# Kernel tuning notes

Measured on AMD Instinct MI355X. Metric: run time of the kernel, lower is better.

Reference implementation:

```python
import jax, jax.numpy as jnp
import numpy as np

BN_EPS = 1e-5
C = 128  # channels (hardcoded by feed_forward convs)


def _bn(v, gamma, beta, mean, var):
    # BatchNorm1d in inference form over channel axis of [B, C, N]
    scale = gamma / jnp.sqrt(var + BN_EPS)
    return (v - mean[:, None]) * scale[:, None] + beta[:, None]


def setup_inputs() -> dict:
    key = jax.random.key(0)
    ks = jax.random.split(key, 8)
    B, N = 8, 2048
    s = 0.05
    return {
        "x": jax.random.normal(ks[0], (B, N, C), jnp.float32),
        "Wq": jax.random.normal(ks[1], (C // 4, C), jnp.float32) * s,
        "Wk": jax.random.normal(ks[2], (C // 4, C), jnp.float32) * s,
        "Wv": jax.random.normal(ks[3], (C, C), jnp.float32) * s,
        "bv": jnp.zeros((C,), jnp.float32),
        "Wt": jax.random.normal(ks[4], (C, C), jnp.float32) * s,
        "bt": jnp.zeros((C,), jnp.float32),
        "g1": jnp.ones((C,), jnp.float32),
        "b1": jnp.zeros((C,), jnp.float32),
        "m1": jnp.zeros((C,), jnp.float32),
        "v1": jnp.ones((C,), jnp.float32),
        "W1": jax.random.normal(ks[5], (512, C), jnp.float32) * s,
        "bf1": jnp.zeros((512,), jnp.float32),
        "W2": jax.random.normal(ks[6], (C, 512), jnp.float32) * s,
        "bf2": jnp.zeros((C,), jnp.float32),
        "g2": jnp.ones((C,), jnp.float32),
        "b2": jnp.zeros((C,), jnp.float32),
        "m2": jnp.zeros((C,), jnp.float32),
        "v2": jnp.ones((C,), jnp.float32),
    }


def reference(x, Wq, Wk, Wv, bv, Wt, bt, g1, b1, m1, v1,
              W1, bf1, W2, bf2, g2, b2, m2, v2):
    # x: [B, N, C] -> work in [B, C, N] layout like the torch module
    xc = jnp.transpose(x, (0, 2, 1))                      # [B, C, N]
    # q_conv(x).permute -> [B, N, C/4]; k_conv -> [B, C/4, N]
    x_q = jnp.einsum('bnc,oc->bno', x, Wq)                # [B, N, C/4]
    x_k = jnp.einsum('bnc,oc->bon', x, Wk)                # [B, C/4, N]
    x_v = jnp.einsum('bnc,oc->bon', x, Wv) + bv[:, None]  # [B, C, N]

    energy = jnp.einsum('bnd,bdm->bnm', x_q, x_k)         # [B, N, N]
    scale = jnp.sqrt(jnp.asarray(C, x.dtype))             # sqrt(x_v.shape[-2])
    attention = jax.nn.softmax(energy / scale, axis=-1)   # [B, N, N]
    x_r = jnp.einsum('bcn,bnm->bcm', x_v, attention)      # [B, C, N]

    t = jnp.einsum('oc,bcn->bon', Wt, xc - x_r) + bt[:, None]
    x_r2 = jax.nn.relu(_bn(t, g1, b1, m1, v1))
    h = xc + x_r2                                         # [B, C, N]

    residual = h
    f = jax.nn.relu(jnp.einsum('oc,bcn->bon', W1, h) + bf1[:, None])
    f = jnp.einsum('of,bfn->bon', W2, f) + bf2[:, None]
    out = _bn(residual + f, g2, b2, m2, v2)               # [B, C, N]
    return jnp.transpose(out, (0, 2, 1))                  # [B, N, C]
```

## Files before the change

kernel.cpp:

```cpp
#include <hip/hip_runtime.h>
#include <hip/hip_bf16.h>

#define BDIM 256
#define NPTS (8 * 2048)
#define CC 128
#define DD 32
#define FF 512
#define NN 2048
#define SCALE 0.08838834764831845f

typedef float f32x4 __attribute__((ext_vector_type(4)));
typedef short s16x8 __attribute__((ext_vector_type(8)));
typedef unsigned short ushort_t;

__device__ __forceinline__ ushort_t bf16r(float x) {
    __hip_bfloat16 h = __float2bfloat16(x);
    return *reinterpret_cast<ushort_t*>(&h);
}
__device__ __forceinline__ float bf16tof(ushort_t u) {
    unsigned v = ((unsigned)u) << 16;
    return *reinterpret_cast<float*>(&v);
}
__device__ __forceinline__ unsigned pack2(float a, float b) {
    return ((unsigned)bf16r(b) << 16) | (unsigned)bf16r(a);
}

__global__ void k_cvt_all(const float* __restrict__ W1, const float* __restrict__ W2,
                          const float* __restrict__ Wq, const float* __restrict__ Wk,
                          const float* __restrict__ Wv, const float* __restrict__ Wt,
                          ushort_t* __restrict__ dst) {
    int i = blockIdx.x * BDIM + threadIdx.x;
    const float* src; int off;
    if (i < 16384)      { src = W1; off = 0; }
    else if (i < 32768) { src = W2; off = 16384; }
    else if (i < 33792) { src = Wq; off = 32768; }
    else if (i < 34816) { src = Wk; off = 33792; }
    else if (i < 38912) { src = Wv; off = 34816; }
    else                { src = Wt; off = 38912; }
    float4 v = ((const float4*)src)[i - off];
    *(uint2*)(dst + (long)i * 4) = make_uint2(pack2(v.x, v.y), pack2(v.z, v.w));
}

__global__ __launch_bounds__(256) void k_proj(
        const float* __restrict__ x, const ushort_t* __restrict__ Wb,
        const float* __restrict__ bv,
        ushort_t* __restrict__ qg, ushort_t* __restrict__ kg,
        ushort_t* __restrict__ vTg) {
    __shared__ ushort_t xs[32][136];
    __shared__ ushort_t qks[32][72];
    __shared__ ushort_t vs[32][136];
    int b = blockIdx.x & 7;
    int n0 = (blockIdx.x >> 3) * 32;
    long base = (long)b * NN + n0;
    int t = threadIdx.x, w = t >> 6, l = t & 63, a = l & 15, g = l >> 4;
    {
        const float4* xg4 = (const float4*)(x + base * CC);
        #pragma unroll
        for (int rep = 0; rep < 4; ++rep) {
            int i = rep * BDIM + t;
            float4 v4 = xg4[i];
            int p = i >> 5, c4 = (i & 31) * 4;
            *(uint2*)&xs[p][c4] = make_uint2(pack2(v4.x, v4.y), pack2(v4.z, v4.w));
        }
    }
    s16x8 bF[3][4];
    #pragma unroll
    for (int ct = 0; ct < 3; ++ct) {
        int ctg = w * 3 + ct;
        #pragma unroll
        for (int ki = 0; ki < 4; ++ki)
            bF[ct][ki] = *(const s16x8*)(Wb + ((long)(ctg * 16 + a)) * CC + ki * 32 + g * 8);
    }
    __syncthreads();
    #pragma unroll
    for (int rt = 0; rt < 2; ++rt) {
        s16x8 aF[4];
        #pragma unroll
        for (int ki = 0; ki < 4; ++ki)
            aF[ki] = *(const s16x8*)&xs[rt * 16 + a][ki * 32 + g * 8];
        #pragma unroll
        for (int ct = 0; ct < 3; ++ct) {
            f32x4 acc = (f32x4){0.f, 0.f, 0.f, 0.f};
            #pragma unroll
            for (int ki = 0; ki < 4; ++ki)
                acc = __builtin_amdgcn_mfma_f32_16x16x32_bf16(aF[ki], bF[ct][ki], acc, 0, 0, 0);
            int ctg = w * 3 + ct;
            int oc = ctg * 16 + a;
            float bias = (oc >= 64) ? bv[oc - 64] : 0.f;
            #pragma unroll
            for (int r = 0; r < 4; ++r) {
                int p = rt * 16 + g * 4 + r;
                float val = acc[r] + bias;
                if (oc < 64) qks[p][oc] = bf16r(val);
                else         vs[p][oc - 64] = bf16r(val);
            }
        }
    }
    __syncthreads();
    {
        int p = t >> 3, c = (t & 7) * 4;
        *(uint2*)(qg + (base + p) * DD + c) = *(const uint2*)&qks[p][c];
        *(uint2*)(kg + (base + p) * DD + c) = *(const uint2*)&qks[p][32 + c];
    }
    #pragma unroll
    for (int rep = 0; rep < 2; ++rep) {
        int i = rep * BDIM + t;
        int c = i & 127, nch = i >> 7;
        int p0 = nch * 8;
        uint4 r;
        r.x = (unsigned)vs[p0+0][c] | ((unsigned)vs[p0+1][c] << 16);
        r.y = (unsigned)vs[p0+2][c] | ((unsigned)vs[p0+3][c] << 16);
        r.z = (unsigned)vs[p0+4][c] | ((unsigned)vs[p0+5][c] << 16);
        r.w = (unsigned)vs[p0+6][c] | ((unsigned)vs[p0+7][c] << 16);
        *(uint4*)(vTg + ((long)(b * CC + c)) * NN + n0 + p0) = r;
    }
}

__global__ __launch_bounds__(256) void k_rowstats(
        const ushort_t* __restrict__ qg, const ushort_t* __restrict__ kg,
        float* __restrict__ rowinv) {
    __shared__ float ps[4][64];
    int b = blockIdx.x & 7;
    int nt = (blockIdx.x >> 3) * 64;
    int t = threadIdx.x, w = t >> 6, l = t & 63, a = l & 15, g = l >> 4;
    s16x8 qA[4];
    #pragma unroll
    for (int s = 0; s < 4; ++s)
        qA[s] = *(const s16x8*)(qg + ((long)(b * NN + nt + s*16 + a)) * DD + g*8);
    float sm[16];
    #pragma unroll
    for (int i = 0; i < 16; ++i) sm[i] = 0.f;
    s16x8 kB = *(const s16x8*)(kg + ((long)(b * NN + w * 16 + a)) * DD + g*8);
    for (int it = 0; it < 32; ++it) {
        s16x8 kBn;
        if (it < 31)
            kBn = *(const s16x8*)(kg + ((long)(b * NN + ((it+1)*4 + w)*16 + a)) * DD + g*8);
        #pragma unroll
        for (int s = 0; s < 4; ++s) {
            f32x4 D = (f32x4){0.f, 0.f, 0.f, 0.f};
            D = __builtin_amdgcn_mfma_f32_16x16x32_bf16(qA[s], kB, D, 0, 0, 0);
            #pragma unroll
            for (int r = 0; r < 4; ++r)
                sm[s * 4 + r] += __expf(D[r] * SCALE);
        }
        kB = kBn;
    }
    #pragma unroll
    for (int off = 1; off < 16; off <<= 1)
        #pragma unroll
        for (int ix = 0; ix < 16; ++ix)
            sm[ix] += __shfl_xor(sm[ix], off, 64);
    if (a == 0) {
        #pragma unroll
        for (int s = 0; s < 4; ++s)
            #pragma unroll
            for (int r = 0; r < 4; ++r)
                ps[w][s * 16 + g * 4 + r] = sm[s * 4 + r];
    }
    __syncthreads();
    if (t < 64) {
        float S = ps[0][t] + ps[1][t] + ps[2][t] + ps[3][t];
        rowinv[(long)b * NN + nt + t] = 1.f / S;
    }
}

__global__ __launch_bounds__(512) void k_pv(
        const ushort_t* __restrict__ qg, const ushort_t* __restrict__ kg,
        const ushort_t* __restrict__ vTg, const float* __restrict__ rowinv,
        const float* __restrict__ x, const ushort_t* __restrict__ Wtb,
        const float* __restrict__ bt,
        const float* __restrict__ g1, const float* __restrict__ b1,
        const float* __restrict__ m1, const float* __restrict__ v1,
        ushort_t* __restrict__ hb) {
    __shared__ __align__(16) char arena[41472];
    auto vTs = (ushort_t (*)[128][72])(arena);
    auto pT  = (ushort_t (*)[72])(arena + 36864);
    int b = blockIdx.x & 7;
    int m0 = (blockIdx.x >> 3) * 32;
    int t = threadIdx.x, w = t >> 6, l = t & 63, a = l & 15, g = l >> 4;
    int nsub = w & 3, msub = w >> 2;
    const ushort_t* vTb = vTg + (long)b * CC * NN;
    s16x8 kf = *(const s16x8*)(kg + ((long)(b * NN + m0 + msub * 16 + a)) * DD + g * 8);
    const ushort_t* qrow = qg + ((long)(b * NN + nsub * 16 + a)) * DD + g * 8;
    const float*    rrow = rowinv + (long)b * NN + nsub * 16 + g * 4;
    int sc = t >> 3;
    int sj = (t & 7) * 8;
    s16x8 qf_c = *(const s16x8*)qrow;
    float4 rr_c = *(const float4*)rrow;
    {
        uint4 v0 = *(const uint4*)(vTb + (long)sc * NN + sj);
        uint4 v1 = *(const uint4*)(vTb + (long)(64 + sc) * NN + sj);
        *(uint4*)&vTs[0][sc][sj] = v0;
        *(uint4*)&vTs[0][64 + sc][sj] = v1;
    }
    f32x4 acc[2];
    acc[0] = (f32x4){0.f, 0.f, 0.f, 0.f};
    acc[1] = (f32x4){0.f, 0.f, 0.f, 0.f};
    int cur = 0;
    __syncthreads();
    s16x8 qf_n; float4 rr_n; uint4 vsr0, vsr1;
    for (int it = 0; it < 32; ++it) {
        long ntn = (long)(it + 1) * 64;
        if (it < 31) {
            vsr0 = *(const uint4*)(vTb + (long)sc * NN + ntn + sj);
            vsr1 = *(const uint4*)(vTb + (long)(64 + sc) * NN + ntn + sj);
            qf_n = *(const s16x8*)(qrow + ntn * DD);
            rr_n = *(const float4*)(rrow + ntn);
        }
        {
            f32x4 e = (f32x4){0.f, 0.f, 0.f, 0.f};
            e = __builtin_amdgcn_mfma_f32_16x16x32_bf16(qf_c, kf, e, 0, 0, 0);
            float p0 = __expf(e[0] * SCALE) * rr_c.x;
            float p1 = __expf(e[1] * SCALE) * rr_c.y;
            float p2 = __expf(e[2] * SCALE) * rr_c.z;
            float p3 = __expf(e[3] * SCALE) * rr_c.w;
            *(uint2*)&pT[msub * 16 + a][nsub * 16 + g * 4] =
                make_uint2(pack2(p0, p1), pack2(p2, p3));
        }
        __syncthreads();
        #pragma unroll
        for (int k2 = 0; k2 < 2; ++k2) {
            s16x8 A0 = *(const s16x8*)&pT[a][k2 * 32 + g * 8];
            s16x8 A1 = *(const s16x8*)&pT[16 + a][k2 * 32 + g * 8];
            s16x8 Bf = *(const s16x8*)&vTs[cur][w * 16 + a][k2 * 32 + g * 8];
            acc[0] = __builtin_amdgcn_mfma_f32_16x16x32_bf16(A0, Bf, acc[0], 0, 0, 0);
            acc[1] = __builtin_amdgcn_mfma_f32_16x16x32_bf16(A1, Bf, acc[1], 0, 0, 0);
        }
        if (it < 31) {
            *(uint4*)&vTs[cur ^ 1][sc][sj] = vsr0;
            *(uint4*)&vTs[cur ^ 1][64 + sc][sj] = vsr1;
        }
        qf_c = qf_n; rr_c = rr_n;
        __syncthreads();
        cur ^= 1;
    }
    auto xb  = (ushort_t (*)[136])(arena);
    auto dsx = (ushort_t (*)[136])(arena + 8704);
    long pbase = (long)b * NN + m0;
    {
        const float4* xg4 = (const float4*)(x + pbase * CC);
        #pragma unroll
        for (int rep = 0; rep < 2; ++rep) {
            int i = rep * 512 + t;
            float4 xv = xg4[i];
            int p = i >> 5, c4 = (i & 31) * 4;
            *(uint2*)&xb[p][c4] = make_uint2(pack2(xv.x, xv.y), pack2(xv.z, xv.w));
        }
    }
    __syncthreads();
    {
        int c = w * 16 + a;
        #pragma unroll
        for (int ms = 0; ms < 2; ++ms)
            #pragma unroll
            for (int r = 0; r < 4; ++r) {
                int ml = ms * 16 + g * 4 + r;
                dsx[ml][c] = bf16r(bf16tof(xb[ml][c]) - acc[ms][r]);
            }
    }
    __syncthreads();
    {
        int ph = w & 1, fh = w >> 1;
        s16x8 aF[4];
        #pragma unroll
        for (int ki = 0; ki < 4; ++ki)
            aF[ki] = *(const s16x8*)&dsx[ph * 16 + a][ki * 32 + g * 8];
        #pragma unroll
        for (int oi = 0; oi < 2; ++oi) {
            int ot = fh * 2 + oi;
            f32x4 ac = (f32x4){0.f, 0.f, 0.f, 0.f};
            #pragma unroll
            for (int ki = 0; ki < 4; ++ki) {
                s16x8 bF = *(const s16x8*)(Wtb + ((long)(ot * 16 + a)) * CC + ki * 32 + g * 8);
                ac = __builtin_amdgcn_mfma_f32_16x16x32_bf16(aF[ki], bF, ac, 0, 0, 0);
            }
            int o = ot * 16 + a;
            float sc = g1[o] * rsqrtf(v1[o] + 1e-5f);
            float mm = m1[o], bb = b1[o], bo = bt[o];
            #pragma unroll
            for (int r = 0; r < 4; ++r) {
                int p = ph * 16 + g * 4 + r;
                float tv = ((ac[r] + bo) - mm) * sc + bb;
                tv = fmaxf(tv, 0.f);
                hb[(pbase + p) * CC + o] = bf16r(bf16tof(xb[p][o]) + tv);
            }
        }
    }
}

__global__ __launch_bounds__(256) void k_ff(
        const ushort_t* __restrict__ hb, const ushort_t* __restrict__ W1b,
        const ushort_t* __restrict__ W2b,
        const float* __restrict__ bf1, const float* __restrict__ bf2,
        const float* __restrict__ g2, const float* __restrict__ b2,
        const float* __restrict__ m2, const float* __restrict__ v2,
        float* __restrict__ out) {
    __shared__ ushort_t hs[32][136];
    __shared__ ushort_t w1s[2][64][128];
    __shared__ ushort_t w2s[2][128][64];
    __shared__ ushort_t fss[32][72];
    long pbase = (long)(blockIdx.x & 7) * NN + (blockIdx.x >> 3) * 32;
    int t = threadIdx.x;
    int l = t & 63, wid = t >> 6;
    int ph = wid & 1, fh = wid >> 1;
    int lr = l & 15, lg = l >> 4;
    for (int i = t; i < 512; i += BDIM) {
        int r = i >> 4, c0 = (i & 15) * 8;
        *(uint4*)&hs[r][c0] = *(const uint4*)(hb + (pbase + r) * CC + c0);
    }
    #pragma unroll
    for (int rep = 0; rep < 4; ++rep) {
        int i = rep * BDIM + t;
        int r = i >> 4, c0 = (i & 15) * 8;
        *(uint4*)&w1s[0][r][c0 ^ ((r & 7) * 8)] = *(const uint4*)(W1b + (long)r * CC + c0);
    }
    #pragma unroll
    for (int rep = 0; rep < 4; ++rep) {
        int i = rep * BDIM + t;
        int r = i >> 3, c0 = (i & 7) * 8;
        *(uint4*)&w2s[0][r][c0 ^ ((r & 7) * 8)] = *(const uint4*)(W2b + (long)r * FF + c0);
    }
    __syncthreads();
    s16x8 hA[4];
    #pragma unroll
    for (int ki = 0; ki < 4; ++ki)
        hA[ki] = *(const s16x8*)&hs[ph * 16 + lr][ki * 32 + lg * 8];
    f32x4 acc2[4];
    #pragma unroll
    for (int i = 0; i < 4; ++i) acc2[i] = (f32x4){0.f, 0.f, 0.f, 0.f};

    int cur = 0;
    uint4 wrg0, wrg1, wrg2, wrg3, wrg4, wrg5, wrg6, wrg7;
    for (int fc = 0; fc < 8; ++fc) {
        if (fc) __syncthreads();
        int f0 = fc * 64;
        if (fc < 7) {
            int f0n = f0 + 64;
            int r1 = t >> 4, c1 = (t & 15) * 8;
            int r2 = t >> 3, c2 = (t & 7) * 8;
            wrg0 = *(const uint4*)(W1b + (long)(f0n + r1) * CC + c1);
            wrg1 = *(const uint4*)(W1b + (long)(f0n + 16 + r1) * CC + c1);
            wrg2 = *(const uint4*)(W1b + (long)(f0n + 32 + r1) * CC + c1);
            wrg3 = *(const uint4*)(W1b + (long)(f0n + 48 + r1) * CC + c1);
            wrg4 = *(const uint4*)(W2b + (long)r2 * FF + f0n + c2);
            wrg5 = *(const uint4*)(W2b + (long)(32 + r2) * FF + f0n + c2);
            wrg6 = *(const uint4*)(W2b + (long)(64 + r2) * FF + f0n + c2);
            wrg7 = *(const uint4*)(W2b + (long)(96 + r2) * FF + f0n + c2);
        }
        #pragma unroll
        for (int fi = 0; fi < 2; ++fi) {
            int ft = fh * 2 + fi;
            int row = ft * 16 + lr;
            f32x4 a1 = (f32x4){0.f, 0.f, 0.f, 0.f};
            #pragma unroll
            for (int ki = 0; ki < 4; ++ki) {
                int col = ki * 32 + lg * 8;
                s16x8 bfr = *(const s16x8*)&w1s[cur][row][col ^ ((row & 7) * 8)];
                a1 = __builtin_amdgcn_mfma_f32_16x16x32_bf16(hA[ki], bfr, a1, 0, 0, 0);
            }
            float bias = bf1[f0 + ft * 16 + lr];
            #pragma unroll
            for (int r = 0; r < 4; ++r) {
                float vv = fmaxf(a1[r] + bias, 0.f);
                fss[ph * 16 + lg * 4 + r][ft * 16 + lr] = bf16r(vv);
            }
        }
        __syncthreads();
        #pragma unroll
        for (int k2 = 0; k2 < 2; ++k2) {
            s16x8 afr = *(const s16x8*)&fss[ph * 16 + lr][k2 * 32 + lg * 8];
            #pragma unroll
            for (int oi = 0; oi < 4; ++oi) {
                int ot = fh * 4 + oi;
                int row = ot * 16 + lr;
                int col = k2 * 32 + lg * 8;
                s16x8 bfr = *(const s16x8*)&w2s[cur][row][col ^ ((row & 7) * 8)];
                acc2[oi] = __builtin_amdgcn_mfma_f32_16x16x32_bf16(afr, bfr, acc2[oi], 0, 0, 0);
            }
        }
        if (fc < 7) {
            int nb = cur ^ 1;
            int r1 = t >> 4, c1 = (t & 15) * 8;
            int r2 = t >> 3, c2 = (t & 7) * 8;
            *(uint4*)&w1s[nb][r1][c1 ^ ((r1 & 7) * 8)] = wrg0;
            *(uint4*)&w1s[nb][16 + r1][c1 ^ ((r1 & 7) * 8)] = wrg1;
            *(uint4*)&w1s[nb][32 + r1][c1 ^ ((r1 & 7) * 8)] = wrg2;
            *(uint4*)&w1s[nb][48 + r1][c1 ^ ((r1 & 7) * 8)] = wrg3;
            *(uint4*)&w2s[nb][r2][c2 ^ ((r2 & 7) * 8)] = wrg4;
            *(uint4*)&w2s[nb][32 + r2][c2 ^ (((32 + r2) & 7) * 8)] = wrg5;
            *(uint4*)&w2s[nb][64 + r2][c2 ^ (((64 + r2) & 7) * 8)] = wrg6;
            *(uint4*)&w2s[nb][96 + r2][c2 ^ (((96 + r2) & 7) * 8)] = wrg7;
            cur = nb;
        }
    }
    #pragma unroll
    for (int oi = 0; oi < 4; ++oi) {
        int o = (fh * 4 + oi) * 16 + lr;
        float sc = g2[o] * rsqrtf(v2[o] + 1e-5f);
        float mm = m2[o], bb = b2[o], bias2 = bf2[o];
        #pragma unroll
        for (int r = 0; r < 4; ++r) {
            int p = ph * 16 + lg * 4 + r;
            float val = bf16tof(hs[p][o]) + acc2[oi][r] + bias2;
            out[(pbase + p) * CC + o] = (val - mm) * sc + bb;
        }
    }
}

extern "C" void kernel_launch(void* const* d_in, const int* in_sizes, int n_in,
                              void* d_out, int out_size, void* d_ws, size_t ws_size,
                              hipStream_t stream) {
    const float* x   = (const float*)d_in[0];
    const float* Wq  = (const float*)d_in[1];
    const float* Wk  = (const float*)d_in[2];
    const float* Wv  = (const float*)d_in[3];
    const float* bv  = (const float*)d_in[4];
    const float* Wt  = (const float*)d_in[5];
    const float* bt  = (const float*)d_in[6];
    const float* g1  = (const float*)d_in[7];
    const float* b1  = (const float*)d_in[8];
    const float* m1  = (const float*)d_in[9];
    const float* v1  = (const float*)d_in[10];
    const float* W1  = (const float*)d_in[11];
    const float* bf1 = (const float*)d_in[12];
    const float* W2  = (const float*)d_in[13];
    const float* bf2 = (const float*)d_in[14];
    const float* g2  = (const float*)d_in[15];
    const float* b2  = (const float*)d_in[16];
    const float* m2  = (const float*)d_in[17];
    const float* v2  = (const float*)d_in[18];
    float* out = (float*)d_out;

    float* ws  = (float*)d_ws;
    float* rin = ws;
    ushort_t* qg   = (ushort_t*)(rin + NPTS);
    ushort_t* kg   = qg + (long)NPTS * DD;
    ushort_t* vTg  = kg + (long)NPTS * DD;
    ushort_t* hbuf = vTg + (long)NPTS * CC;
    ushort_t* W1b  = hbuf + (long)NPTS * CC;
    ushort_t* W2b  = W1b + FF * CC;
    ushort_t* Wb   = W2b + FF * CC;
    ushort_t* Wtb  = Wb + 192 * CC;

    k_cvt_all<<<168, BDIM, 0, stream>>>(W1, W2, Wq, Wk, Wv, Wt, W1b);
    k_proj<<<NPTS / 32, BDIM, 0, stream>>>(x, Wb, bv, qg, kg, vTg);
    k_rowstats<<<8 * (NN / 64), BDIM, 0, stream>>>(qg, kg, rin);
    k_pv<<<8 * (NN / 32), 512, 0, stream>>>(qg, kg, vTg, rin,
                                            x, Wtb, bt, g1, b1, m1, v1, hbuf);
    k_ff<<<NPTS / 32, BDIM, 0, stream>>>(hbuf, W1b, W2b, bf1, bf2, g2, b2, m2, v2, out);
}
```

Before: 70.41 us.

## Halve k_pv output tile and warp-specialize softmax vs V-tile loading

```diff
diff --git a/kernel.cpp b/kernel.cpp
--- a/kernel.cpp
+++ b/kernel.cpp
@@ -172,118 +172,107 @@
         const float* __restrict__ g1, const float* __restrict__ b1,
         const float* __restrict__ m1, const float* __restrict__ v1,
         ushort_t* __restrict__ hb) {
-    __shared__ __align__(16) char arena[41472];
+    __shared__ __align__(16) char arena[39168];
     auto vTs = (ushort_t (*)[128][72])(arena);
     auto pT  = (ushort_t (*)[72])(arena + 36864);
     int b = blockIdx.x & 7;
-    int m0 = (blockIdx.x >> 3) * 32;
+    int m0 = (blockIdx.x >> 3) * 16;
     int t = threadIdx.x, w = t >> 6, l = t & 63, a = l & 15, g = l >> 4;
-    int nsub = w & 3, msub = w >> 2;
+    int nsub = w & 3;
     const ushort_t* vTb = vTg + (long)b * CC * NN;
-    s16x8 kf = *(const s16x8*)(kg + ((long)(b * NN + m0 + msub * 16 + a)) * DD + g * 8);
+    s16x8 kf = *(const s16x8*)(kg + ((long)(b * NN + m0 + a)) * DD + g * 8);
     const ushort_t* qrow = qg + ((long)(b * NN + nsub * 16 + a)) * DD + g * 8;
     const float*    rrow = rowinv + (long)b * NN + nsub * 16 + g * 4;
-    int sc = t >> 3;
-    int sj = (t & 7) * 8;
-    s16x8 qf_c = *(const s16x8*)qrow;
-    float4 rr_c = *(const float4*)rrow;
-    {
-        uint4 v0 = *(const uint4*)(vTb + (long)sc * NN + sj);
-        uint4 v1 = *(const uint4*)(vTb + (long)(64 + sc) * NN + sj);
-        *(uint4*)&vTs[0][sc][sj] = v0;
-        *(uint4*)&vTs[0][64 + sc][sj] = v1;
-    }
-    f32x4 acc[2];
-    acc[0] = (f32x4){0.f, 0.f, 0.f, 0.f};
-    acc[1] = (f32x4){0.f, 0.f, 0.f, 0.f};
+    int ts = t & 255;
+    int sc = ts >> 3;
+    int sj = (ts & 7) * 8;
+    {
+        int pc = t >> 3;
+        int pj = (t & 7) * 8;
+        *(uint4*)&vTs[0][pc][pj]      = *(const uint4*)(vTb + (long)pc * NN + pj);
+        *(uint4*)&vTs[0][64 + pc][pj] = *(const uint4*)(vTb + (long)(64 + pc) * NN + pj);
+    }
+    s16x8 qf_c; float4 rr_c;
+    if (w < 4) { qf_c = *(const s16x8*)qrow; rr_c = *(const float4*)rrow; }
+    f32x4 acc = (f32x4){0.f, 0.f, 0.f, 0.f};
     int cur = 0;
     __syncthreads();
-    s16x8 qf_n; float4 rr_n; uint4 vsr0, vsr1;
+    s16x8 qf_n; float4 rr_n; uint4 vsr[4];
     for (int it = 0; it < 32; ++it) {
         long ntn = (long)(it + 1) * 64;
-        if (it < 31) {
-            vsr0 = *(const uint4*)(vTb + (long)sc * NN + ntn + sj);
-            vsr1 = *(const uint4*)(vTb + (long)(64 + sc) * NN + ntn + sj);
-            qf_n = *(const s16x8*)(qrow + ntn * DD);
-            rr_n = *(const float4*)(rrow + ntn);
-        }
-        {
+        if (w < 4) {
             f32x4 e = (f32x4){0.f, 0.f, 0.f, 0.f};
             e = __builtin_amdgcn_mfma_f32_16x16x32_bf16(qf_c, kf, e, 0, 0, 0);
             float p0 = __expf(e[0] * SCALE) * rr_c.x;
             float p1 = __expf(e[1] * SCALE) * rr_c.y;
             float p2 = __expf(e[2] * SCALE) * rr_c.z;
             float p3 = __expf(e[3] * SCALE) * rr_c.w;
-            *(uint2*)&pT[msub * 16 + a][nsub * 16 + g * 4] =
+            *(uint2*)&pT[a][nsub * 16 + g * 4] =
                 make_uint2(pack2(p0, p1), pack2(p2, p3));
+            if (it < 31) {
+                qf_n = *(const s16x8*)(qrow + ntn * DD);
+                rr_n = *(const float4*)(rrow + ntn);
+            }
+        } else if (it < 31) {
+            #pragma unroll
+            for (int rep = 0; rep < 4; ++rep)
+                vsr[rep] = *(const uint4*)(vTb + (long)(sc + rep * 32) * NN + ntn + sj);
         }
         __syncthreads();
         #pragma unroll
         for (int k2 = 0; k2 < 2; ++k2) {
             s16x8 A0 = *(const s16x8*)&pT[a][k2 * 32 + g * 8];
-            s16x8 A1 = *(const s16x8*)&pT[16 + a][k2 * 32 + g * 8];
             s16x8 Bf = *(const s16x8*)&vTs[cur][w * 16 + a][k2 * 32 + g * 8];
-            acc[0] = __builtin_amdgcn_mfma_f32_16x16x32_bf16(A0, Bf, acc[0], 0, 0, 0);
-            acc[1] = __builtin_amdgcn_mfma_f32_16x16x32_bf16(A1, Bf, acc[1], 0, 0, 0);
-        }
-        if (it < 31) {
-            *(uint4*)&vTs[cur ^ 1][sc][sj] = vsr0;
-            *(uint4*)&vTs[cur ^ 1][64 + sc][sj] = vsr1;
-        }
-        qf_c = qf_n; rr_c = rr_n;
+            acc = __builtin_amdgcn_mfma_f32_16x16x32_bf16(A0, Bf, acc, 0, 0, 0);
+        }
+        if (w >= 4 && it < 31) {
+            #pragma unroll
+            for (int rep = 0; rep < 4; ++rep)
+                *(uint4*)&vTs[cur ^ 1][sc + rep * 32][sj] = vsr[rep];
+        }
+        if (w < 4) { qf_c = qf_n; rr_c = rr_n; }
         __syncthreads();
         cur ^= 1;
     }
     auto xb  = (ushort_t (*)[136])(arena);
-    auto dsx = (ushort_t (*)[136])(arena + 8704);
+    auto dsx = (ushort_t (*)[136])(arena + 4352);
     long pbase = (long)b * NN + m0;
     {
         const float4* xg4 = (const float4*)(x + pbase * CC);
-        #pragma unroll
-        for (int rep = 0; rep < 2; ++rep) {
-            int i = rep * 512 + t;
-            float4 xv = xg4[i];
-            int p = i >> 5, c4 = (i & 31) * 4;
-            *(uint2*)&xb[p][c4] = make_uint2(pack2(xv.x, xv.y), pack2(xv.z, xv.w));
-        }
+        float4 xv = xg4[t];
+        int p = t >> 5, c4 = (t & 31) * 4;
+        *(uint2*)&xb[p][c4] = make_uint2(pack2(xv.x, xv.y), pack2(xv.z, xv.w));
     }
     __syncthreads();
     {
         int c = w * 16 + a;
         #pragma unroll
-        for (int ms = 0; ms < 2; ++ms)
-            #pragma unroll
-            for (int r = 0; r < 4; ++r) {
-                int ml = ms * 16 + g * 4 + r;
-                dsx[ml][c] = bf16r(bf16tof(xb[ml][c]) - acc[ms][r]);
-            }
-    }
-    __syncthreads();
-    {
-        int ph = w & 1, fh = w >> 1;
+        for (int r = 0; r < 4; ++r) {
+            int ml = g * 4 + r;
+            dsx[ml][c] = bf16r(bf16tof(xb[ml][c]) - acc[r]);
+        }
+    }
+    __syncthreads();
+    {
         s16x8 aF[4];
         #pragma unroll
         for (int ki = 0; ki < 4; ++ki)
-            aF[ki] = *(const s16x8*)&dsx[ph * 16 + a][ki * 32 + g * 8];
-        #pragma unroll
-        for (int oi = 0; oi < 2; ++oi) {
-            int ot = fh * 2 + oi;
-            f32x4 ac = (f32x4){0.f, 0.f, 0.f, 0.f};
-            #pragma unroll
-            for (int ki = 0; ki < 4; ++ki) {
-                s16x8 bF = *(const s16x8*)(Wtb + ((long)(ot * 16 + a)) * CC + ki * 32 + g * 8);
-                ac = __builtin_amdgcn_mfma_f32_16x16x32_bf16(aF[ki], bF, ac, 0, 0, 0);
-            }
-            int o = ot * 16 + a;
-            float sc = g1[o] * rsqrtf(v1[o] + 1e-5f);
-            float mm = m1[o], bb = b1[o], bo = bt[o];
-            #pragma unroll
-            for (int r = 0; r < 4; ++r) {
-                int p = ph * 16 + g * 4 + r;
-                float tv = ((ac[r] + bo) - mm) * sc + bb;
-                tv = fmaxf(tv, 0.f);
-                hb[(pbase + p) * CC + o] = bf16r(bf16tof(xb[p][o]) + tv);
-            }
+            aF[ki] = *(const s16x8*)&dsx[a][ki * 32 + g * 8];
+        f32x4 ac = (f32x4){0.f, 0.f, 0.f, 0.f};
+        #pragma unroll
+        for (int ki = 0; ki < 4; ++ki) {
+            s16x8 bF = *(const s16x8*)(Wtb + ((long)(w * 16 + a)) * CC + ki * 32 + g * 8);
+            ac = __builtin_amdgcn_mfma_f32_16x16x32_bf16(aF[ki], bF, ac, 0, 0, 0);
+        }
+        int o = w * 16 + a;
+        float sc2 = g1[o] * rsqrtf(v1[o] + 1e-5f);
+        float mm = m1[o], bb = b1[o], bo = bt[o];
+        #pragma unroll
+        for (int r = 0; r < 4; ++r) {
+            int p = g * 4 + r;
+            float tv = ((ac[r] + bo) - mm) * sc2 + bb;
+            tv = fmaxf(tv, 0.f);
+            hb[(pbase + p) * CC + o] = bf16r(bf16tof(xb[p][o]) + tv);
         }
     }
 }
@@ -445,7 +434,7 @@
     k_cvt_all<<<168, BDIM, 0, stream>>>(W1, W2, Wq, Wk, Wv, Wt, W1b);
     k_proj<<<NPTS / 32, BDIM, 0, stream>>>(x, Wb, bv, qg, kg, vTg);
     k_rowstats<<<8 * (NN / 64), BDIM, 0, stream>>>(qg, kg, rin);
-    k_pv<<<8 * (NN / 32), 512, 0, stream>>>(qg, kg, vTg, rin,
+    k_pv<<<8 * (NN / 16), 512, 0, stream>>>(qg, kg, vTg, rin,
                                             x, Wtb, bt, g1, b1, m1, v1, hbuf);
     k_ff<<<NPTS / 32, BDIM, 0, stream>>>(hbuf, W1b, W2b, bf1, bf2, g2, b2, m2, v2, out);
 }
```

After: 183.2 us. 2.6x slower.
